# Performance work log

Hardware: AMD Instinct MI355X
Metric: run time of the kernel (lower is better)

Reference implementation:

```python
import jax, jax.numpy as jnp
import numpy as np

N_HEADS = 32
KV_HEADS = 8
HEAD_DIM = 128
D_MODEL = 4096
CLIP_QKV = 8.0
ROPE_THETA = 500000.0


def setup_inputs() -> dict:
    key = jax.random.key(0)
    k1, k2, k3 = jax.random.split(key, 3)
    x = jax.random.normal(k1, (2, 2048, D_MODEL), dtype=jnp.float32)
    Wqkv = jax.random.normal(k2, ((KV_HEADS * 2 + N_HEADS) * HEAD_DIM, D_MODEL), dtype=jnp.float32) * (D_MODEL ** -0.5)
    Wout = jax.random.normal(k3, (D_MODEL, D_MODEL), dtype=jnp.float32) * (D_MODEL ** -0.5)
    return {"x": x, "Wqkv": Wqkv, "Wout": Wout}


def _rope(t):
    # t: [B, H, L, D]; half-split (non-traditional) RoPE, offset=0
    B, H, L, D = t.shape
    half = D // 2
    inv_freq = 1.0 / (ROPE_THETA ** (jnp.arange(0, half, dtype=jnp.float32) / half))
    angles = jnp.arange(L, dtype=jnp.float32)[:, None] * inv_freq[None, :]  # [L, half]
    cos = jnp.cos(angles)[None, None]  # [1,1,L,half]
    sin = jnp.sin(angles)[None, None]
    t1, t2 = t[..., :half], t[..., half:]
    return jnp.concatenate([t1 * cos - t2 * sin, t2 * cos + t1 * sin], axis=-1).astype(t.dtype)


def reference(x, Wqkv, Wout):
    B, L, D = x.shape
    qkv = jnp.clip(x @ Wqkv.T, -CLIP_QKV, CLIP_QKV)
    q = qkv[..., :D_MODEL]
    k = qkv[..., D_MODEL:D_MODEL + KV_HEADS * HEAD_DIM]
    v = qkv[..., D_MODEL + KV_HEADS * HEAD_DIM:]
    q = q.reshape(B, L, N_HEADS, HEAD_DIM).transpose(0, 2, 1, 3)   # [B,H,L,d]
    k = k.reshape(B, L, KV_HEADS, HEAD_DIM).transpose(0, 2, 1, 3)  # [B,Hkv,L,d]
    v = v.reshape(B, L, KV_HEADS, HEAD_DIM).transpose(0, 2, 1, 3)
    q = _rope(q)
    k = _rope(k)
    # GQA: broadcast kv heads to query heads
    rep = N_HEADS // KV_HEADS
    k = jnp.repeat(k, rep, axis=1)  # [B,H,L,d]
    v = jnp.repeat(v, rep, axis=1)
    scale = HEAD_DIM ** -0.5
    scores = jnp.einsum('bhqd,bhkd->bhqk', q, k) * scale
    causal = jnp.tril(jnp.ones((L, L), dtype=bool))
    scores = jnp.where(causal[None, None], scores, jnp.finfo(scores.dtype).min)
    probs = jax.nn.softmax(scores, axis=-1)
    out = jnp.einsum('bhqk,bhkd->bhqd', probs, v)
    out = out.transpose(0, 2, 1, 3).reshape(B, L, D_MODEL)
    return out @ Wout.T
```

## Files before the change

kernel.cpp:

```cpp
#include <hip/hip_runtime.h>
#include <hip/hip_bf16.h>
#include <math.h>

typedef __hip_bfloat16 bf16;
typedef __attribute__((ext_vector_type(8))) short bf16x8;
typedef __attribute__((ext_vector_type(4))) short bf16x4;
typedef __attribute__((ext_vector_type(4))) float f32x4;

__device__ __forceinline__ void glds16(const bf16* g, bf16* l) {
    __builtin_amdgcn_global_load_lds(
        (const __attribute__((address_space(1))) void*)g,
        (__attribute__((address_space(3))) void*)l, 16, 0, 0);
}

__global__ __launch_bounds__(256)
void convert_to_bf16(const void* __restrict__ src, bf16* __restrict__ dst, long n) {
    const unsigned short* u16 = (const unsigned short*)src;
    int lane = threadIdx.x & 63;
    unsigned short u = u16[lane * 2];
    int e = (u >> 7) & 0xFF;
    int isf32 = __popcll(__ballot(e >= 0x86)) > 4;
    long i = ((long)blockIdx.x * 256 + threadIdx.x) * 8;
    if (i >= n) return;
    if (isf32) {
        const float* s = (const float*)src;
        bf16x8 o;
        #pragma unroll
        for (int j = 0; j < 8; j++) {
            bf16 b = (bf16)s[i + j];
            o[j] = *(short*)&b;
        }
        *(bf16x8*)(dst + i) = o;
    } else {
        *(bf16x8*)(dst + i) = *(const bf16x8*)((const bf16*)src + i);
    }
}

template<bool CLIP, typename OUT>
__global__ __launch_bounds__(256)
void gemm_bt(const bf16* __restrict__ A, const bf16* __restrict__ B,
             OUT* __restrict__ C, int M, int N, int K) {
    __shared__ __align__(16) bf16 sA[128 * 32];
    __shared__ __align__(16) bf16 sB[128 * 32];
    const int tid  = threadIdx.x;
    const int lane = tid & 63;
    const int wave = tid >> 6;
    const int wm   = wave >> 1;
    const int wn   = wave & 1;
    const int row  = lane & 15;
    const int quad = lane >> 4;
    const int bn = blockIdx.x, bm = blockIdx.y;

    const int r  = tid >> 2;
    const int kc = (tid & 3) * 8;
    const bf16* gA = A + (size_t)(bm * 128 + r) * K + kc;
    const bf16* gB = B + (size_t)(bn * 128 + r) * K + kc;
    bf16* lA = sA + tid * 8;
    bf16* lB = sB + tid * 8;

    f32x4 acc[4][4] = {};

    for (int kt = 0; kt < K; kt += 32) {
        glds16(gA + kt,                    lA);
        glds16(gA + kt + (size_t)64 * K,   lA + 2048);
        glds16(gB + kt,                    lB);
        glds16(gB + kt + (size_t)64 * K,   lB + 2048);
        __syncthreads();
        bf16x8 af[4], bfr[4];
        #pragma unroll
        for (int mt = 0; mt < 4; mt++)
            af[mt] = *(const bf16x8*)(sA + (wm * 64 + mt * 16 + row) * 32 + quad * 8);
        #pragma unroll
        for (int nt = 0; nt < 4; nt++)
            bfr[nt] = *(const bf16x8*)(sB + (wn * 64 + nt * 16 + row) * 32 + quad * 8);
        #pragma unroll
        for (int mt = 0; mt < 4; mt++)
            #pragma unroll
            for (int nt = 0; nt < 4; nt++)
                acc[mt][nt] = __builtin_amdgcn_mfma_f32_16x16x32_bf16(
                    af[mt], bfr[nt], acc[mt][nt], 0, 0, 0);
        __syncthreads();
    }

    #pragma unroll
    for (int mt = 0; mt < 4; mt++) {
        #pragma unroll
        for (int nt = 0; nt < 4; nt++) {
            #pragma unroll
            for (int v = 0; v < 4; v++) {
                float val = acc[mt][nt][v];
                if (CLIP) val = fminf(fmaxf(val, -8.0f), 8.0f);
                int grow = bm * 128 + wm * 64 + mt * 16 + quad * 4 + v;
                int gcol = bn * 128 + wn * 64 + nt * 16 + row;
                C[(size_t)grow * N + gcol] = (OUT)val;
            }
        }
    }
}

__global__ __launch_bounds__(256)
void rope_reorder(const bf16* __restrict__ qkv, bf16* __restrict__ Q,
                  bf16* __restrict__ Kd, bf16* __restrict__ VT) {
    const int token = blockIdx.y;
    const int slot  = blockIdx.x * 4 + (threadIdx.x >> 6);
    const int lane  = threadIdx.x & 63;
    const int b = token >> 11, l = token & 2047;
    const bf16* src = qkv + (size_t)token * 6144 + slot * 128;
    if (slot < 40) {
        float x1 = __bfloat162float(src[lane]);
        float x2 = __bfloat162float(src[lane + 64]);
        float inv_freq = powf(500000.0f, -(float)lane * (1.0f / 64.0f));
        float ang = (float)l * inv_freq;
        float s, c;
        sincosf(ang, &s, &c);
        float o1 = x1 * c - x2 * s;
        float o2 = x2 * c + x1 * s;
        bf16* dst;
        if (slot < 32) dst = Q  + ((size_t)(b * 32 + slot)        * 2048 + l) * 128;
        else           dst = Kd + ((size_t)(b * 8  + (slot - 32)) * 2048 + l) * 128;
        dst[lane]      = (bf16)o1;
        dst[lane + 64] = (bf16)o2;
    } else {
        bf16* dst = VT + (size_t)(b * 8 + (slot - 40)) * 128 * 2048 + l;
        dst[(size_t)lane * 2048]        = src[lane];
        dst[(size_t)(lane + 64) * 2048] = src[lane + 64];
    }
}

#define SP_STR 72

__global__ __launch_bounds__(256, 3)
void attn_kernel(const bf16* __restrict__ Q, const bf16* __restrict__ K,
                 const bf16* __restrict__ V, bf16* __restrict__ Oout) {
    const int qt = 31 - blockIdx.x;
    const int bh = blockIdx.y;
    const int b = bh >> 5, h = bh & 31;
    const int kh = h >> 2;
    const bf16* Qp = Q + ((size_t)(b * 32 + h) * 2048 + qt * 64) * 128;
    const bf16* Kp = K + (size_t)(b * 8 + kh) * 2048 * 128;
    const bf16* Vp = V + (size_t)(b * 8 + kh) * 128 * 2048;

    __shared__ __align__(16) bf16 sK[64 * 128];
    __shared__ __align__(16) bf16 sV[128 * 64];
    __shared__ __align__(16) bf16 sP[4 * 16 * SP_STR];

    const int tid = threadIdx.x, lane = tid & 63, wave = tid >> 6;
    const int row = lane & 15, quad = lane >> 4;
    const int rx  = (row & 7) << 4;
    char* sKb = (char*)sK;
    char* sVb = (char*)sV;

    const int krow = tid >> 4;
    const int kc8  = (tid & 15) ^ (krow & 7);
    const int vrow = tid >> 3;
    const int vc8  = (tid & 7) ^ (vrow & 7);
    const int ldst = tid * 16;

    bf16x8 aq[4];
    #pragma unroll
    for (int kk = 0; kk < 4; kk++)
        aq[kk] = *(const bf16x8*)(Qp + (size_t)(wave * 16 + row) * 128 + (kk * 4 + quad) * 8);

    bf16x8 kpf[4], vpf[4];
    #pragma unroll
    for (int j = 0; j < 4; j++) {
        kpf[j] = *(const bf16x8*)(Kp + (size_t)(j * 16 + krow) * 128 + kc8 * 8);
        vpf[j] = *(const bf16x8*)(Vp + (size_t)(j * 32 + vrow) * 2048 + vc8 * 8);
    }
    #pragma unroll
    for (int j = 0; j < 4; j++) {
        *(bf16x8*)(sKb + ldst + j * 4096) = kpf[j];
        *(bf16x8*)(sVb + ldst + j * 4096) = vpf[j];
    }
    __syncthreads();

    float pm = -1e30f, pl = 0.0f;
    f32x4 o_acc[8] = {};
    const float scale = 0.08838834764831845f;

    for (int jj = 0; jj <= qt; jj++) {
        if (jj < qt) {
            #pragma unroll
            for (int j = 0; j < 4; j++) {
                kpf[j] = *(const bf16x8*)(Kp + (size_t)((jj + 1) * 64 + j * 16 + krow) * 128 + kc8 * 8);
                vpf[j] = *(const bf16x8*)(Vp + (size_t)(j * 32 + vrow) * 2048 + (jj + 1) * 64 + vc8 * 8);
            }
        }

        f32x4 s_acc[4] = {};
        __builtin_amdgcn_s_setprio(1);
        #pragma unroll
        for (int nt = 0; nt < 4; nt++) {
            #pragma unroll
            for (int kk = 0; kk < 4; kk++) {
                bf16x8 bk = *(const bf16x8*)(sKb + (nt * 16 + row) * 256
                                             + (((kk * 4 + quad) * 16) ^ rx));
                s_acc[nt] = __builtin_amdgcn_mfma_f32_16x16x32_bf16(
                    bk, aq[kk], s_acc[nt], 0, 0, 0);
            }
        }
        __builtin_amdgcn_s_setprio(0);

        #pragma unroll
        for (int nt = 0; nt < 4; nt++) {
            #pragma unroll
            for (int v = 0; v < 4; v++) {
                float s = s_acc[nt][v] * scale;
                if (jj == qt) {
                    int kpos = nt * 16 + quad * 4 + v;
                    int qrow = wave * 16 + row;
                    if (kpos > qrow) s = -1e30f;
                }
                s_acc[nt][v] = s;
            }
        }
        float m_loc = s_acc[0][0];
        #pragma unroll
        for (int nt = 0; nt < 4; nt++)
            #pragma unroll
            for (int v = 0; v < 4; v++)
                m_loc = fmaxf(m_loc, s_acc[nt][v]);
        m_loc = fmaxf(m_loc, __shfl_xor(m_loc, 16, 64));
        m_loc = fmaxf(m_loc, __shfl_xor(m_loc, 32, 64));

        if (!__all(m_loc - pm <= 8.0f)) {
            float mn = fmaxf(pm, m_loc);
            float al = __expf(pm - mn);
            pm = mn;
            pl *= al;
            float al_q[4];
            #pragma unroll
            for (int v = 0; v < 4; v++)
                al_q[v] = __shfl(al, quad * 4 + v, 64);
            #pragma unroll
            for (int dt = 0; dt < 8; dt++)
                #pragma unroll
                for (int v = 0; v < 4; v++)
                    o_acc[dt][v] *= al_q[v];
        }

        float rs = 0.0f;
        #pragma unroll
        for (int nt = 0; nt < 4; nt++) {
            bf16x4 pw;
            #pragma unroll
            for (int v = 0; v < 4; v++) {
                float p = __expf(s_acc[nt][v] - pm);
                rs += p;
                bf16 pb = (bf16)p;
                pw[v] = *(short*)&pb;
            }
            *(bf16x4*)(sP + (wave * 16 + row) * SP_STR + nt * 16 + quad * 4) = pw;
        }
        rs += __shfl_xor(rs, 16, 64);
        rs += __shfl_xor(rs, 32, 64);
        pl += rs;

        __builtin_amdgcn_s_setprio(1);
        #pragma unroll
        for (int kk = 0; kk < 2; kk++) {
            bf16x8 pa = *(const bf16x8*)(sP + (wave * 16 + row) * SP_STR + (kk * 4 + quad) * 8);
            #pragma unroll
            for (int dt = 0; dt < 8; dt++) {
                bf16x8 vb = *(const bf16x8*)(sVb + (dt * 16 + row) * 128
                                             + (((kk * 4 + quad) * 16) ^ rx));
                o_acc[dt] = __builtin_amdgcn_mfma_f32_16x16x32_bf16(
                    pa, vb, o_acc[dt], 0, 0, 0);
            }
        }
        __builtin_amdgcn_s_setprio(0);

        if (jj < qt) {
            __syncthreads();
            #pragma unroll
            for (int j = 0; j < 4; j++) {
                *(bf16x8*)(sKb + ldst + j * 4096) = kpf[j];
                *(bf16x8*)(sVb + ldst + j * 4096) = vpf[j];
            }
            __syncthreads();
        }
    }

    float pl_q[4];
    #pragma unroll
    for (int v = 0; v < 4; v++)
        pl_q[v] = __shfl(pl, quad * 4 + v, 64);
    const int token = b * 2048 + qt * 64 + wave * 16;
    #pragma unroll
    for (int dt = 0; dt < 8; dt++) {
        #pragma unroll
        for (int v = 0; v < 4; v++) {
            float o = o_acc[dt][v] / pl_q[v];
            int trow = token + quad * 4 + v;
            Oout[(size_t)trow * 4096 + h * 128 + dt * 16 + row] = (bf16)o;
        }
    }
}

extern "C" void kernel_launch(void* const* d_in, const int* in_sizes, int n_in,
                              void* d_out, int out_size, void* d_ws, size_t ws_size,
                              hipStream_t stream) {
    float* out = (float*)d_out;

    const size_t MB = 1024 * 1024;
    char* ws = (char*)d_ws;
    bf16* xb    = (bf16*)(ws);
    bf16* Wqkvb = (bf16*)(ws + 32 * MB);
    bf16* qkv   = (bf16*)(ws + 80 * MB);
    bf16* Qb    = (bf16*)(ws + 32 * MB);
    bf16* Kb    = (bf16*)(ws + 64 * MB);
    bf16* VTb   = (bf16*)(ws + 72 * MB);
    bf16* Woutb = (bf16*)(ws + 80 * MB);
    bf16* attn  = xb;

    convert_to_bf16<<<8192,  256, 0, stream>>>(d_in[0], xb,    16777216L);
    convert_to_bf16<<<12288, 256, 0, stream>>>(d_in[1], Wqkvb, 25165824L);
    gemm_bt<true, bf16><<<dim3(48, 32), 256, 0, stream>>>(xb, Wqkvb, qkv, 4096, 6144, 4096);
    rope_reorder<<<dim3(12, 4096), 256, 0, stream>>>(qkv, Qb, Kb, VTb);
    convert_to_bf16<<<8192,  256, 0, stream>>>(d_in[2], Woutb, 16777216L);
    attn_kernel<<<dim3(32, 64), 256, 0, stream>>>(Qb, Kb, VTb, attn);
    gemm_bt<false, float><<<dim3(32, 32), 256, 0, stream>>>(attn, Woutb, out, 4096, 4096, 4096);
}
```

Before: 948.8 us.

## Replace GEMM with 256x256 double-buffered, swizzled-LDS kernel and XCD block remap

Both projection GEMMs move from a 128x128 tile, 256-thread kernel to a 256x256 tile, 512-thread kernel with K-step 64. The new kernel double-buffers LDS so the global_load_lds for the next tile overlaps the MFMAs, XOR-swizzles LDS chunks to avoid bank conflicts, and remaps block IDs across the 8 XCDs for L2 locality. The aim is higher arithmetic intensity and hiding load latency. The cost is more LDS (128KB) and more registers, which limits occupancy, and few workgroups: 384 and 256 on 256 CUs, which risks tail imbalance.

```diff
diff --git a/kernel.cpp b/kernel.cpp
--- a/kernel.cpp
+++ b/kernel.cpp
@@ -37,61 +37,119 @@
 }
 
 template<bool CLIP, typename OUT>
-__global__ __launch_bounds__(256)
-void gemm_bt(const bf16* __restrict__ A, const bf16* __restrict__ B,
+__global__ __launch_bounds__(512, 2)
+void gemm256(const bf16* __restrict__ A, const bf16* __restrict__ B,
              OUT* __restrict__ C, int M, int N, int K) {
-    __shared__ __align__(16) bf16 sA[128 * 32];
-    __shared__ __align__(16) bf16 sB[128 * 32];
-    const int tid  = threadIdx.x;
-    const int lane = tid & 63;
-    const int wave = tid >> 6;
-    const int wm   = wave >> 1;
-    const int wn   = wave & 1;
-    const int row  = lane & 15;
-    const int quad = lane >> 4;
-    const int bn = blockIdx.x, bm = blockIdx.y;
-
-    const int r  = tid >> 2;
-    const int kc = (tid & 3) * 8;
-    const bf16* gA = A + (size_t)(bm * 128 + r) * K + kc;
-    const bf16* gB = B + (size_t)(bn * 128 + r) * K + kc;
-    bf16* lA = sA + tid * 8;
-    bf16* lB = sB + tid * 8;
-
-    f32x4 acc[4][4] = {};
-
-    for (int kt = 0; kt < K; kt += 32) {
-        glds16(gA + kt,                    lA);
-        glds16(gA + kt + (size_t)64 * K,   lA + 2048);
-        glds16(gB + kt,                    lB);
-        glds16(gB + kt + (size_t)64 * K,   lB + 2048);
-        __syncthreads();
-        bf16x8 af[4], bfr[4];
-        #pragma unroll
-        for (int mt = 0; mt < 4; mt++)
-            af[mt] = *(const bf16x8*)(sA + (wm * 64 + mt * 16 + row) * 32 + quad * 8);
-        #pragma unroll
-        for (int nt = 0; nt < 4; nt++)
-            bfr[nt] = *(const bf16x8*)(sB + (wn * 64 + nt * 16 + row) * 32 + quad * 8);
-        #pragma unroll
-        for (int mt = 0; mt < 4; mt++)
-            #pragma unroll
-            for (int nt = 0; nt < 4; nt++)
-                acc[mt][nt] = __builtin_amdgcn_mfma_f32_16x16x32_bf16(
-                    af[mt], bfr[nt], acc[mt][nt], 0, 0, 0);
-        __syncthreads();
-    }
-
-    #pragma unroll
-    for (int mt = 0; mt < 4; mt++) {
-        #pragma unroll
-        for (int nt = 0; nt < 4; nt++) {
+    __shared__ __align__(16) bf16 sA[2][256 * 64];
+    __shared__ __align__(16) bf16 sB[2][256 * 64];
+
+    const int tid   = threadIdx.x;
+    const int lane  = tid & 63;
+    const int row16 = lane & 15;
+    const int quad  = lane >> 4;
+    const int wid   = tid >> 6;
+    const int wr    = wid >> 2;
+    const int wc    = wid & 3;
+
+    const int nwg  = gridDim.x * gridDim.y;
+    const int orig = blockIdx.y * gridDim.x + blockIdx.x;
+    const int cpx  = nwg >> 3;
+    const int sw   = (orig & 7) * cpx + (orig >> 3);
+    const int bn   = sw % gridDim.x;
+    const int bm   = sw / gridDim.x;
+
+    const int srow   = tid >> 3;
+    const int schunk = (tid & 7) ^ (srow & 7);
+    const bf16* gA = A + (size_t)(bm * 256) * K + schunk * 8;
+    const bf16* gB = B + (size_t)(bn * 256) * K + schunk * 8;
+
+    #define STAGE256(u, t)                                                     \
+        do {                                                                   \
+            _Pragma("unroll")                                                  \
+            for (int q = 0; q < 4; q++) {                                      \
+                glds16(gA + (size_t)(q * 64 + srow) * K + (t) * 64,            \
+                       &sA[u][0] + q * 4096 + tid * 8);                        \
+                glds16(gB + (size_t)(q * 64 + srow) * K + (t) * 64,            \
+                       &sB[u][0] + q * 4096 + tid * 8);                        \
+            }                                                                  \
+        } while (0)
+
+    const int cx0 = ((quad) ^ (row16 & 7)) << 4;
+    const int cx1 = ((4 + quad) ^ (row16 & 7)) << 4;
+    const int aRowOff = (wr * 128 + row16) * 128;
+    const int bRowOff = (wc * 64 + row16) * 128;
+
+    f32x4 acc[8][4] = {};
+
+    const int NT = K >> 6;
+    STAGE256(0, 0);
+    STAGE256(1, 1);
+
+    for (int t = 0; t < NT; t++) {
+        const int cur = t & 1;
+        if (t + 1 < NT) {
+            asm volatile("s_waitcnt vmcnt(8)" ::: "memory");
+        } else {
+            asm volatile("s_waitcnt vmcnt(0)" ::: "memory");
+        }
+        __builtin_amdgcn_s_barrier();
+        __builtin_amdgcn_sched_barrier(0);
+
+        const char* aRd = (const char*)(&sA[cur][0]) + aRowOff;
+        const char* bRd = (const char*)(&sB[cur][0]) + bRowOff;
+
+        bf16x8 af0[8], bf0[4];
+        #pragma unroll
+        for (int i = 0; i < 8; i++)
+            af0[i] = *(const bf16x8*)(aRd + i * 2048 + cx0);
+        #pragma unroll
+        for (int j = 0; j < 4; j++)
+            bf0[j] = *(const bf16x8*)(bRd + j * 2048 + cx0);
+        asm volatile("s_waitcnt lgkmcnt(0)" ::: "memory");
+        __builtin_amdgcn_sched_barrier(0);
+        __builtin_amdgcn_s_setprio(1);
+        #pragma unroll
+        for (int i = 0; i < 8; i++)
+            #pragma unroll
+            for (int j = 0; j < 4; j++)
+                acc[i][j] = __builtin_amdgcn_mfma_f32_16x16x32_bf16(
+                    af0[i], bf0[j], acc[i][j], 0, 0, 0);
+        __builtin_amdgcn_s_setprio(0);
+        __builtin_amdgcn_sched_barrier(0);
+
+        bf16x8 af1[8], bf1[4];
+        #pragma unroll
+        for (int i = 0; i < 8; i++)
+            af1[i] = *(const bf16x8*)(aRd + i * 2048 + cx1);
+        #pragma unroll
+        for (int j = 0; j < 4; j++)
+            bf1[j] = *(const bf16x8*)(bRd + j * 2048 + cx1);
+        asm volatile("s_waitcnt lgkmcnt(0)" ::: "memory");
+        __builtin_amdgcn_sched_barrier(0);
+        __builtin_amdgcn_s_barrier();
+        if (t + 2 < NT) STAGE256(cur, t + 2);
+
+        __builtin_amdgcn_s_setprio(1);
+        #pragma unroll
+        for (int i = 0; i < 8; i++)
+            #pragma unroll
+            for (int j = 0; j < 4; j++)
+                acc[i][j] = __builtin_amdgcn_mfma_f32_16x16x32_bf16(
+                    af1[i], bf1[j], acc[i][j], 0, 0, 0);
+        __builtin_amdgcn_s_setprio(0);
+    }
+    #undef STAGE256
+
+    #pragma unroll
+    for (int i = 0; i < 8; i++) {
+        #pragma unroll
+        for (int j = 0; j < 4; j++) {
             #pragma unroll
             for (int v = 0; v < 4; v++) {
-                float val = acc[mt][nt][v];
+                float val = acc[i][j][v];
                 if (CLIP) val = fminf(fmaxf(val, -8.0f), 8.0f);
-                int grow = bm * 128 + wm * 64 + mt * 16 + quad * 4 + v;
-                int gcol = bn * 128 + wn * 64 + nt * 16 + row;
+                int grow = bm * 256 + wr * 128 + i * 16 + quad * 4 + v;
+                int gcol = bn * 256 + wc * 64 + j * 16 + row16;
                 C[(size_t)grow * N + gcol] = (OUT)val;
             }
         }
@@ -315,9 +373,9 @@
 
     convert_to_bf16<<<8192,  256, 0, stream>>>(d_in[0], xb,    16777216L);
     convert_to_bf16<<<12288, 256, 0, stream>>>(d_in[1], Wqkvb, 25165824L);
-    gemm_bt<true, bf16><<<dim3(48, 32), 256, 0, stream>>>(xb, Wqkvb, qkv, 4096, 6144, 4096);
+    gemm256<true, bf16><<<dim3(24, 16), 512, 0, stream>>>(xb, Wqkvb, qkv, 4096, 6144, 4096);
     rope_reorder<<<dim3(12, 4096), 256, 0, stream>>>(qkv, Qb, Kb, VTb);
     convert_to_bf16<<<8192,  256, 0, stream>>>(d_in[2], Woutb, 16777216L);
     attn_kernel<<<dim3(32, 64), 256, 0, stream>>>(Qb, Kb, VTb, attn);
-    gemm_bt<false, float><<<dim3(32, 32), 256, 0, stream>>>(attn, Woutb, out, 4096, 4096, 4096);
-}
+    gemm256<false, float><<<dim3(16, 16), 512, 0, stream>>>(attn, Woutb, out, 4096, 4096, 4096);
+}
```

New measurement: 845.4 us. -10.9%, faster.
